# Optimization experiments

Measured on AMD Instinct MI355X. Metric: run time of the kernel, lower is better.

## Reference

```python
import jax, jax.numpy as jnp
import numpy as np

B, S, D = 2, 2048, 2048
H = 16
KV_RANK, Q_RANK = 512, 1536
NOPE, ROPE_D, VD = 128, 64, 128
QK_D = NOPE + ROPE_D  # 192


def _rope(t, positions):
    # t: (B, H, S, d) with d even; rotate-half RoPE, theta=10000
    d = t.shape[-1]
    inv_freq = 1.0 / (10000.0 ** (jnp.arange(0, d, 2, dtype=jnp.float32) / d))
    ang = positions.astype(jnp.float32)[:, None] * inv_freq  # (S, d//2)
    cos, sin = jnp.cos(ang), jnp.sin(ang)                    # (S, d//2)
    t1, t2 = t[..., : d // 2], t[..., d // 2 :]
    return jnp.concatenate([t1 * cos - t2 * sin, t2 * cos + t1 * sin], axis=-1)


def setup_inputs() -> dict:
    key = jax.random.key(0)
    ks = jax.random.split(key, 10)
    sc = 0.02
    return {
        "x": jax.random.normal(ks[0], (B, S, D), dtype=jnp.float32),
        "positions": jnp.arange(S, dtype=jnp.int32),
        # torch.nn.Linear weights are (out_features, in_features)
        "Wq_down": jax.random.normal(ks[1], (Q_RANK, D), dtype=jnp.float32) * sc,
        "Wq_up": jax.random.normal(ks[2], (H * NOPE, Q_RANK), dtype=jnp.float32) * sc,
        "Wq_rope": jax.random.normal(ks[3], (H * ROPE_D, Q_RANK), dtype=jnp.float32) * sc,
        "Wkv_down": jax.random.normal(ks[4], (KV_RANK, D), dtype=jnp.float32) * sc,
        "Wk_up": jax.random.normal(ks[5], (H * NOPE, KV_RANK), dtype=jnp.float32) * sc,
        "Wv_up": jax.random.normal(ks[6], (H * VD, KV_RANK), dtype=jnp.float32) * sc,
        "Wk_rope": jax.random.normal(ks[7], (ROPE_D, D), dtype=jnp.float32) * sc,
        "Wo": jax.random.normal(ks[8], (D, H * VD), dtype=jnp.float32) * sc,
    }


def reference(x, positions, Wq_down, Wq_up, Wq_rope, Wkv_down, Wk_up, Wv_up, Wk_rope, Wo):
    bsz, seq_len, _ = x.shape

    # Query path: low-rank down, then nope + rope up-projections
    c_q = x @ Wq_down.T                                             # (B, S, Q_RANK)
    q_c = (c_q @ Wq_up.T).reshape(bsz, seq_len, H, NOPE).transpose(0, 2, 1, 3)
    q_r = (c_q @ Wq_rope.T).reshape(bsz, seq_len, H, ROPE_D).transpose(0, 2, 1, 3)
    q_r = _rope(q_r, positions)
    q = jnp.concatenate([q_c, q_r], axis=-1)                        # (B, H, S, QK_D)

    # KV path: shared latent, single rope head broadcast to all heads
    c_kv = x @ Wkv_down.T                                           # (B, S, KV_RANK)
    k_c = (c_kv @ Wk_up.T).reshape(bsz, seq_len, H, NOPE).transpose(0, 2, 1, 3)
    v_c = (c_kv @ Wv_up.T).reshape(bsz, seq_len, H, VD).transpose(0, 2, 1, 3)
    k_r = (x @ Wk_rope.T).reshape(bsz, seq_len, 1, ROPE_D).transpose(0, 2, 1, 3)
    k_r = _rope(k_r, positions)
    k_r = jnp.broadcast_to(k_r, (bsz, H, seq_len, ROPE_D))
    k = jnp.concatenate([k_c, k_r], axis=-1)                        # (B, H, S, QK_D)

    # Causal SDPA, scale = 1/sqrt(total qk head dim)
    scale = 1.0 / math.sqrt(QK_D) if False else QK_D ** -0.5
    scores = jnp.einsum("bhqd,bhkd->bhqk", q, k) * scale
    causal = jnp.tril(jnp.ones((seq_len, seq_len), dtype=bool))
    scores = jnp.where(causal, scores, jnp.finfo(scores.dtype).min)
    attn = jax.nn.softmax(scores, axis=-1)
    out = jnp.einsum("bhqk,bhkd->bhqd", attn, v_c)                  # (B, H, S, VD)

    out = out.transpose(0, 2, 1, 3).reshape(bsz, seq_len, H * VD)
    return out @ Wo.T                                               # (B, S, D)
```

## Files before the change

### kernel.cpp

```cpp
#include <hip/hip_runtime.h>
#include <cmath>

#define SLEN 2048

typedef __bf16 bf16x8 __attribute__((ext_vector_type(8)));
typedef float  f32x4  __attribute__((ext_vector_type(4)));

__device__ inline void gld16(const void* g, void* l) {
    __builtin_amdgcn_global_load_lds(
        (const __attribute__((address_space(1))) void*)(uintptr_t)g,
        (__attribute__((address_space(3))) void*)(unsigned)(uintptr_t)l, 16, 0, 0);
}

struct CvArgs {
    const float* src[9];
    __bf16*      dst[9];
    long         cum[10];
};
__global__ __launch_bounds__(256)
void convert_all(CvArgs a) {
    long i8 = ((long)blockIdx.x * 256 + threadIdx.x) * 8;
    if (i8 >= a.cum[9]) return;
    int s = 0;
#pragma unroll
    for (int k = 1; k < 9; k++) if (i8 >= a.cum[k]) s = k;
    long loc = i8 - a.cum[s];
    const float* sp = a.src[s] + loc;
    float4 u0 = *(const float4*)(sp);
    float4 u1 = *(const float4*)(sp + 4);
    bf16x8 o;
    o[0] = (__bf16)u0.x; o[1] = (__bf16)u0.y; o[2] = (__bf16)u0.z; o[3] = (__bf16)u0.w;
    o[4] = (__bf16)u1.x; o[5] = (__bf16)u1.y; o[6] = (__bf16)u1.z; o[7] = (__bf16)u1.w;
    *(bf16x8*)(a.dst[s] + loc) = o;
}

struct Outs { __bf16* a; __bf16* b; __bf16* c; float* f; };

__global__ __launch_bounds__(256, 2)
void gemm_nt(const __bf16* __restrict__ A, const __bf16* __restrict__ B,
             Outs o, const int* __restrict__ positions,
             int M, int N, int K, int mode, float scale) {
    __shared__ __bf16 As[128 * 64];
    __shared__ __bf16 Bs[128 * 64];
    int tid = threadIdx.x;
    int wave = tid >> 6, lane = tid & 63;
    int lane15 = lane & 15, quad = lane >> 4;
    int ri = lane >> 3, ci = lane & 7;
    int cg = ci ^ ri;
    int m0 = blockIdx.x * 128, n0 = blockIdx.y * 128;
    int wm = (wave & 1) * 64, wn = (wave >> 1) * 64;
    f32x4 acc[4][4] = {};

    for (int k0 = 0; k0 < K; k0 += 64) {
#pragma unroll
        for (int t = 0; t < 4; t++) {
            int rr = wave * 32 + t * 8;
            int r = rr + ri;
            gld16(A + (size_t)(m0 + r) * K + k0 + cg * 8, As + rr * 64);
            int br = n0 + r; if (br > N - 1) br = N - 1;
            gld16(B + (size_t)br * K + k0 + cg * 8, Bs + rr * 64);
        }
        __syncthreads();
#pragma unroll
        for (int kk = 0; kk < 64; kk += 32) {
            int jb = kk >> 3;
            bf16x8 af[4], bfr[4];
#pragma unroll
            for (int mt = 0; mt < 4; mt++) {
                int rA = wm + mt * 16 + lane15;
                af[mt] = *(bf16x8*)(As + rA * 64 + (((jb + quad) ^ (rA & 7)) << 3));
            }
#pragma unroll
            for (int nt = 0; nt < 4; nt++) {
                int rB = wn + nt * 16 + lane15;
                bfr[nt] = *(bf16x8*)(Bs + rB * 64 + (((jb + quad) ^ (rB & 7)) << 3));
            }
#pragma unroll
            for (int mt = 0; mt < 4; mt++)
#pragma unroll
                for (int nt = 0; nt < 4; nt++)
                    acc[mt][nt] = __builtin_amdgcn_mfma_f32_16x16x32_bf16(
                        af[mt], bfr[nt], acc[mt][nt], 0, 0, 0);
        }
        __syncthreads();
    }

    const float KLOG = 13.287712379549449f / 32.0f;

    if (mode == 8 && n0 == 2048) {
        if (wn == 0) {
#pragma unroll
            for (int mt = 0; mt < 4; mt++) {
                int row = m0 + wm + mt * 16 + quad * 4;
#pragma unroll
                for (int nt = 0; nt < 2; nt++) {
                    int i = nt * 16 + lane15;
                    float inv = exp2f(-(float)i * KLOG);
#pragma unroll
                    for (int r = 0; r < 4; r++) {
                        int tok = row + r;
                        float p = (float)positions[tok & (SLEN - 1)];
                        float sn, cs; sincosf(p * inv, &sn, &cs);
                        float t1 = acc[mt][nt][r], t2 = acc[mt][nt + 2][r];
                        float rot1 = t1 * cs - t2 * sn;
                        float rot2 = t2 * cs + t1 * sn;
                        size_t ob = (size_t)tok * 3072 + 128;
#pragma unroll
                        for (int hh = 0; hh < 16; hh++) {
                            o.c[ob + hh * 192 + i]      = (__bf16)rot1;
                            o.c[ob + hh * 192 + 32 + i] = (__bf16)rot2;
                        }
                    }
                }
            }
        }
        return;
    }
    if (mode == 9 && n0 >= 2048) {
        int hh = (n0 + wn - 2048) >> 6;
#pragma unroll
        for (int mt = 0; mt < 4; mt++) {
            int row = m0 + wm + mt * 16 + quad * 4;
#pragma unroll
            for (int nt = 0; nt < 2; nt++) {
                int i = nt * 16 + lane15;
                float inv = exp2f(-(float)i * KLOG);
#pragma unroll
                for (int r = 0; r < 4; r++) {
                    int tok = row + r;
                    float p = (float)positions[tok & (SLEN - 1)];
                    float sn, cs; sincosf(p * inv, &sn, &cs);
                    float t1 = acc[mt][nt][r], t2 = acc[mt][nt + 2][r];
                    size_t ob = (size_t)tok * 3072 + hh * 192 + 128;
                    o.a[ob + i]      = (__bf16)((t1 * cs - t2 * sn) * scale);
                    o.a[ob + 32 + i] = (__bf16)((t2 * cs + t1 * sn) * scale);
                }
            }
        }
        return;
    }

#pragma unroll
    for (int mt = 0; mt < 4; mt++) {
        int row = m0 + wm + mt * 16 + quad * 4;
#pragma unroll
        for (int nt = 0; nt < 4; nt++) {
            int col = n0 + wn + nt * 16 + lane15;
            if (col < N) {
#pragma unroll
                for (int r = 0; r < 4; r++) {
                    float v = acc[mt][nt][r];
                    size_t rw = (size_t)(row + r);
                    if (mode == 2) {
                        o.f[rw * N + col] = v;
                    } else if (mode == 8) {
                        if (col < 1536) o.a[rw * 1536 + col] = (__bf16)v;
                        else            o.b[rw * 512 + col - 1536] = (__bf16)v;
                    } else if (mode == 9) {
                        o.a[rw * 3072 + (col >> 7) * 192 + (col & 127)] =
                            (__bf16)(v * scale);
                    } else {
                        if (col < 2048)
                            o.a[rw * 3072 + (col >> 7) * 192 + (col & 127)] = (__bf16)v;
                        else {
                            int d = col - 2048;
                            o.b[((size_t)d * 2 + (rw >> 11)) * 2048 + (rw & 2047)] = (__bf16)v;
                        }
                    }
                }
            }
        }
    }
}

__global__ __launch_bounds__(256, 2)
void mla_attn(const __bf16* __restrict__ Q, const __bf16* __restrict__ K,
              const __bf16* __restrict__ Vt, __bf16* __restrict__ O) {
    __shared__ __bf16 Ks[64 * 192];
    __shared__ __bf16 Vs[128 * 64];
    __shared__ __bf16 Ps[4][32][72];
    int tid = threadIdx.x, wave = tid >> 6, lane = tid & 63;
    int lane15 = lane & 15, quad = lane >> 4;
    int h = blockIdx.y, b = blockIdx.z;
    int x = blockIdx.x;
    int qt0 = (x & 1) ? (x >> 1) : (15 - (x >> 1));
    int qt = b ? (15 - qt0) : qt0;
    int q0 = qt * 128;
    const __bf16* Qb  = Q + (size_t)b * SLEN * 3072 + h * 192;
    const __bf16* Kb  = K + (size_t)b * SLEN * 3072 + h * 192;
    const __bf16* vtb = Vt + ((size_t)(h * 128) * 2 + b) * 2048;

    bf16x8 qf[2][6];
#pragma unroll
    for (int mt = 0; mt < 2; mt++) {
        int qrow = q0 + wave * 32 + mt * 16 + lane15;
#pragma unroll
        for (int kk = 0; kk < 6; kk++)
            qf[mt][kk] = *(const bf16x8*)(Qb + (size_t)qrow * 3072 + kk * 32 + quad * 8);
    }
    bf16x8 ones;
#pragma unroll
    for (int e = 0; e < 8; e++) ones[e] = (__bf16)1.0f;

    f32x4 o_acc[2][8] = {};
    float m_i[2][4], l_i[2][4];
#pragma unroll
    for (int mt = 0; mt < 2; mt++)
#pragma unroll
        for (int r = 0; r < 4; r++) { m_i[mt][r] = -3.0e38f; l_i[mt][r] = 0.0f; }

    for (int j0 = 0; j0 <= q0 + 64; j0 += 64) {
#pragma unroll
        for (int t = 0; t < 6; t++) {
            int sb = (wave * 6 + t) * 64;
            int slot = sb + lane;
            int r = slot / 24;
            int c = slot - r * 24;
            int cgk = (c & ~7) | ((c & 7) ^ (r & 7));
            gld16(Kb + (size_t)(j0 + r) * 3072 + cgk * 8, Ks + sb * 8);
        }
#pragma unroll
        for (int t = 0; t < 4; t++) {
            int sb = (wave * 4 + t) * 64;
            int slot = sb + lane;
            int r = slot >> 3, c = slot & 7;
            gld16(vtb + (size_t)r * 4096 + j0 + (c ^ (r & 7)) * 8, Vs + sb * 8);
        }
        __syncthreads();

        f32x4 acc[2][4] = {};
#pragma unroll
        for (int kk = 0; kk < 6; kk++) {
#pragma unroll
            for (int nt = 0; nt < 4; nt++) {
                int n = nt * 16 + lane15;
                int j = kk * 4 + quad;
                int cl = (j & ~7) | ((j & 7) ^ (n & 7));
                bf16x8 kf = *(bf16x8*)(Ks + n * 192 + cl * 8);
#pragma unroll
                for (int mt = 0; mt < 2; mt++)
                    acc[mt][nt] = __builtin_amdgcn_mfma_f32_16x16x32_bf16(
                        qf[mt][kk], kf, acc[mt][nt], 0, 0, 0);
            }
        }

        if (j0 >= q0) {
#pragma unroll
            for (int mt = 0; mt < 2; mt++) {
                int rowg = q0 + wave * 32 + mt * 16 + quad * 4;
#pragma unroll
                for (int nt = 0; nt < 4; nt++) {
                    int colg = j0 + nt * 16 + lane15;
#pragma unroll
                    for (int r = 0; r < 4; r++)
                        if (colg > rowg + r) acc[mt][nt][r] = -3.0e38f;
                }
            }
        }

        float mx[2][4];
        bool need = false;
#pragma unroll
        for (int mt = 0; mt < 2; mt++)
#pragma unroll
            for (int r = 0; r < 4; r++) {
                float v = fmaxf(fmaxf(acc[mt][0][r], acc[mt][1][r]),
                                fmaxf(acc[mt][2][r], acc[mt][3][r]));
                mx[mt][r] = v;
                need = need || (v > m_i[mt][r] + 24.0f);
            }
        if (__any(need)) {
#pragma unroll
            for (int mt = 0; mt < 2; mt++)
#pragma unroll
                for (int r = 0; r < 4; r++) {
                    float v = mx[mt][r];
#pragma unroll
                    for (int d = 8; d >= 1; d >>= 1) v = fmaxf(v, __shfl_xor(v, d));
                    float mn = fmaxf(m_i[mt][r], v);
                    float alpha = exp2f(m_i[mt][r] - mn);
                    m_i[mt][r] = mn;
                    l_i[mt][r] *= alpha;
#pragma unroll
                    for (int nt = 0; nt < 8; nt++) o_acc[mt][nt][r] *= alpha;
                }
        }

#pragma unroll
        for (int mt = 0; mt < 2; mt++)
#pragma unroll
            for (int r = 0; r < 4; r++)
#pragma unroll
                for (int nt = 0; nt < 4; nt++) {
                    float pp = exp2f(acc[mt][nt][r] - m_i[mt][r]);
                    Ps[wave][mt * 16 + quad * 4 + r][nt * 16 + lane15] = (__bf16)pp;
                }

        f32x4 rs[2] = {};
#pragma unroll
        for (int ks = 0; ks < 2; ks++) {
            bf16x8 pf[2];
#pragma unroll
            for (int mt = 0; mt < 2; mt++)
                pf[mt] = *(bf16x8*)(&Ps[wave][mt * 16 + lane15][ks * 32 + quad * 8]);
#pragma unroll
            for (int nt = 0; nt < 8; nt++) {
                int nn = nt * 16 + lane15;
                int j = ks * 4 + quad;
                bf16x8 vf = *(bf16x8*)(Vs + nn * 64 + (j ^ (nn & 7)) * 8);
#pragma unroll
                for (int mt = 0; mt < 2; mt++)
                    o_acc[mt][nt] = __builtin_amdgcn_mfma_f32_16x16x32_bf16(
                        pf[mt], vf, o_acc[mt][nt], 0, 0, 0);
            }
#pragma unroll
            for (int mt = 0; mt < 2; mt++)
                rs[mt] = __builtin_amdgcn_mfma_f32_16x16x32_bf16(
                    pf[mt], ones, rs[mt], 0, 0, 0);
        }
#pragma unroll
        for (int mt = 0; mt < 2; mt++)
#pragma unroll
            for (int r = 0; r < 4; r++) l_i[mt][r] += rs[mt][r];
        __syncthreads();
    }

    int tokb = b * SLEN + q0 + wave * 32 + quad * 4;
#pragma unroll
    for (int mt = 0; mt < 2; mt++) {
#pragma unroll
        for (int r = 0; r < 4; r++) {
            float inv_l = 1.0f / l_i[mt][r];
            int tok = tokb + mt * 16 + r;
#pragma unroll
            for (int nt = 0; nt < 8; nt++) {
                O[(size_t)tok * 2048 + h * 128 + nt * 16 + lane15] =
                    (__bf16)(o_acc[mt][nt][r] * inv_l);
            }
        }
    }
}

extern "C" void kernel_launch(void* const* d_in, const int* in_sizes, int n_in,
                              void* d_out, int out_size, void* d_ws, size_t ws_size,
                              hipStream_t stream) {
    (void)in_sizes; (void)n_in; (void)out_size; (void)ws_size;
    const int* pos = (const int*)d_in[1];
    float* out = (float*)d_out;

    char* ws = (char*)d_ws;
    size_t off = 0;
    auto alloc = [&](size_t bytes) {
        char* p = ws + off;
        off += (bytes + 255) & ~(size_t)255;
        return p;
    };
    __bf16* x_bf  = (__bf16*)alloc(8388608ull * 2);
    __bf16* Wcat1 = (__bf16*)alloc(4325376ull * 2);
    __bf16* Wcat2 = (__bf16*)alloc(4718592ull * 2);
    __bf16* Wcat3 = (__bf16*)alloc(4194304ull * 2);
    __bf16* Wob   = (__bf16*)alloc(4194304ull * 2);
    __bf16* c_q   = (__bf16*)alloc(4096ull * 1536 * 2);
    __bf16* c_kv  = (__bf16*)alloc(4096ull * 512 * 2);
    __bf16* v_t   = (__bf16*)alloc(4096ull * 2048 * 2);
    __bf16* q_all = (__bf16*)alloc(4096ull * 3072 * 2);
    __bf16* k_all = (__bf16*)alloc(4096ull * 3072 * 2);
    __bf16* attn_o = (__bf16*)c_q;

    const float scale_l2 = 1.4426950408889634f / sqrtf(192.0f);
    dim3 blk(256);

    CvArgs cv;
    cv.src[0] = (const float*)d_in[0]; cv.dst[0] = x_bf;
    cv.src[1] = (const float*)d_in[2]; cv.dst[1] = Wcat1;
    cv.src[2] = (const float*)d_in[5]; cv.dst[2] = Wcat1 + 3145728;
    cv.src[3] = (const float*)d_in[8]; cv.dst[3] = Wcat1 + 4194304;
    cv.src[4] = (const float*)d_in[3]; cv.dst[4] = Wcat2;
    cv.src[5] = (const float*)d_in[4]; cv.dst[5] = Wcat2 + 3145728;
    cv.src[6] = (const float*)d_in[6]; cv.dst[6] = Wcat3;
    cv.src[7] = (const float*)d_in[7]; cv.dst[7] = Wcat3 + 1048576;
    cv.src[8] = (const float*)d_in[9]; cv.dst[8] = Wob;
    long ns[9] = {8388608, 3145728, 1048576, 131072, 3145728, 1572864,
                  1048576, 1048576, 4194304};
    cv.cum[0] = 0;
    for (int i = 0; i < 9; i++) cv.cum[i + 1] = cv.cum[i] + ns[i];
    convert_all<<<dim3((unsigned)(cv.cum[9] / 2048)), blk, 0, stream>>>(cv);

    Outs o1 = { c_q, c_kv, k_all, nullptr };
    gemm_nt<<<dim3(32, 17), blk, 0, stream>>>(x_bf, Wcat1, o1, pos, 4096, 2112, 2048, 8, 1.0f);
    Outs o2 = { q_all, nullptr, nullptr, nullptr };
    gemm_nt<<<dim3(32, 24), blk, 0, stream>>>(c_q, Wcat2, o2, pos, 4096, 3072, 1536, 9, scale_l2);
    Outs o3 = { k_all, v_t, nullptr, nullptr };
    gemm_nt<<<dim3(32, 32), blk, 0, stream>>>(c_kv, Wcat3, o3, pos, 4096, 4096, 512, 10, 1.0f);
    mla_attn<<<dim3(16, 16, 2), blk, 0, stream>>>(q_all, k_all, v_t, attn_o);
    Outs o4 = { nullptr, nullptr, nullptr, out };
    gemm_nt<<<dim3(32, 16), blk, 0, stream>>>(attn_o, Wob, o4, pos, 4096, 2048, 2048, 2, 1.0f);
}
```

Before: 419.8 us.

## Double-buffer K/V tiles and pair causal query tiles per attention block

The attention kernel now double-buffers K and V in shared memory, prefetching the next 64-key tile while the current one is computed, and uses vmcnt waits with raw barriers in place of a full __syncthreads per tile. Each block processes two query tiles (x and 15-x) so every block gets an equal amount of causal work, and the grid is halved. Launch bounds drop to one block per CU, because the doubled LDS use and the extra registers cost occupancy that the prefetch is meant to make up for.

```diff
diff --git a/kernel.cpp b/kernel.cpp
--- a/kernel.cpp
+++ b/kernel.cpp
@@ -173,43 +173,25 @@
     }
 }
 
-__global__ __launch_bounds__(256, 2)
+__global__ __launch_bounds__(256, 1)
 void mla_attn(const __bf16* __restrict__ Q, const __bf16* __restrict__ K,
               const __bf16* __restrict__ Vt, __bf16* __restrict__ O) {
-    __shared__ __bf16 Ks[64 * 192];
-    __shared__ __bf16 Vs[128 * 64];
+    __shared__ __bf16 Ks[2][64 * 192];
+    __shared__ __bf16 Vs[2][128 * 64];
     __shared__ __bf16 Ps[4][32][72];
     int tid = threadIdx.x, wave = tid >> 6, lane = tid & 63;
     int lane15 = lane & 15, quad = lane >> 4;
     int h = blockIdx.y, b = blockIdx.z;
     int x = blockIdx.x;
-    int qt0 = (x & 1) ? (x >> 1) : (15 - (x >> 1));
-    int qt = b ? (15 - qt0) : qt0;
-    int q0 = qt * 128;
     const __bf16* Qb  = Q + (size_t)b * SLEN * 3072 + h * 192;
     const __bf16* Kb  = K + (size_t)b * SLEN * 3072 + h * 192;
     const __bf16* vtb = Vt + ((size_t)(h * 128) * 2 + b) * 2048;
 
-    bf16x8 qf[2][6];
-#pragma unroll
-    for (int mt = 0; mt < 2; mt++) {
-        int qrow = q0 + wave * 32 + mt * 16 + lane15;
-#pragma unroll
-        for (int kk = 0; kk < 6; kk++)
-            qf[mt][kk] = *(const bf16x8*)(Qb + (size_t)qrow * 3072 + kk * 32 + quad * 8);
-    }
     bf16x8 ones;
 #pragma unroll
     for (int e = 0; e < 8; e++) ones[e] = (__bf16)1.0f;
 
-    f32x4 o_acc[2][8] = {};
-    float m_i[2][4], l_i[2][4];
-#pragma unroll
-    for (int mt = 0; mt < 2; mt++)
-#pragma unroll
-        for (int r = 0; r < 4; r++) { m_i[mt][r] = -3.0e38f; l_i[mt][r] = 0.0f; }
-
-    for (int j0 = 0; j0 <= q0 + 64; j0 += 64) {
+    auto stage = [&](int j0, int buf) {
 #pragma unroll
         for (int t = 0; t < 6; t++) {
             int sb = (wave * 6 + t) * 64;
@@ -217,125 +199,166 @@
             int r = slot / 24;
             int c = slot - r * 24;
             int cgk = (c & ~7) | ((c & 7) ^ (r & 7));
-            gld16(Kb + (size_t)(j0 + r) * 3072 + cgk * 8, Ks + sb * 8);
+            gld16(Kb + (size_t)(j0 + r) * 3072 + cgk * 8, &Ks[buf][0] + sb * 8);
         }
 #pragma unroll
         for (int t = 0; t < 4; t++) {
             int sb = (wave * 4 + t) * 64;
             int slot = sb + lane;
             int r = slot >> 3, c = slot & 7;
-            gld16(vtb + (size_t)r * 4096 + j0 + (c ^ (r & 7)) * 8, Vs + sb * 8);
-        }
-        __syncthreads();
-
-        f32x4 acc[2][4] = {};
-#pragma unroll
-        for (int kk = 0; kk < 6; kk++) {
-#pragma unroll
-            for (int nt = 0; nt < 4; nt++) {
-                int n = nt * 16 + lane15;
-                int j = kk * 4 + quad;
-                int cl = (j & ~7) | ((j & 7) ^ (n & 7));
-                bf16x8 kf = *(bf16x8*)(Ks + n * 192 + cl * 8);
+            gld16(vtb + (size_t)r * 4096 + j0 + (c ^ (r & 7)) * 8, &Vs[buf][0] + sb * 8);
+        }
+    };
+
+    for (int pass = 0; pass < 2; pass++) {
+        int qt = pass ? (15 - x) : x;
+        int q0 = qt * 128;
+
+        bf16x8 qf[2][6];
+#pragma unroll
+        for (int mt = 0; mt < 2; mt++) {
+            int qrow = q0 + wave * 32 + mt * 16 + lane15;
+#pragma unroll
+            for (int kk = 0; kk < 6; kk++)
+                qf[mt][kk] = *(const bf16x8*)(Qb + (size_t)qrow * 3072 + kk * 32 + quad * 8);
+        }
+
+        f32x4 o_acc[2][8] = {};
+        float m_i[2][4], l_i[2][4];
+#pragma unroll
+        for (int mt = 0; mt < 2; mt++)
+#pragma unroll
+            for (int r = 0; r < 4; r++) { m_i[mt][r] = -3.0e38f; l_i[mt][r] = 0.0f; }
+
+        int ntiles = 2 * qt + 2;
+        stage(0, 0);
+
+        for (int t = 0; t < ntiles; t++) {
+            int cur = t & 1;
+            if (t + 1 < ntiles) {
+                stage((t + 1) * 64, cur ^ 1);
+                asm volatile("s_waitcnt vmcnt(10)" ::: "memory");
+            } else {
+                asm volatile("s_waitcnt vmcnt(0)" ::: "memory");
+            }
+            __builtin_amdgcn_sched_barrier(0);
+            __builtin_amdgcn_s_barrier();
+            __builtin_amdgcn_sched_barrier(0);
+
+            const __bf16* Ksc = &Ks[cur][0];
+            const __bf16* Vsc = &Vs[cur][0];
+            int j0 = t * 64;
+
+            f32x4 acc[2][4] = {};
+#pragma unroll
+            for (int kk = 0; kk < 6; kk++) {
+#pragma unroll
+                for (int nt = 0; nt < 4; nt++) {
+                    int n = nt * 16 + lane15;
+                    int j = kk * 4 + quad;
+                    int cl = (j & ~7) | ((j & 7) ^ (n & 7));
+                    bf16x8 kf = *(bf16x8*)(Ksc + n * 192 + cl * 8);
+#pragma unroll
+                    for (int mt = 0; mt < 2; mt++)
+                        acc[mt][nt] = __builtin_amdgcn_mfma_f32_16x16x32_bf16(
+                            qf[mt][kk], kf, acc[mt][nt], 0, 0, 0);
+                }
+            }
+
+            if (j0 >= q0) {
+#pragma unroll
+                for (int mt = 0; mt < 2; mt++) {
+                    int rowg = q0 + wave * 32 + mt * 16 + quad * 4;
+#pragma unroll
+                    for (int nt = 0; nt < 4; nt++) {
+                        int colg = j0 + nt * 16 + lane15;
+#pragma unroll
+                        for (int r = 0; r < 4; r++)
+                            if (colg > rowg + r) acc[mt][nt][r] = -3.0e38f;
+                    }
+                }
+            }
+
+            float mx[2][4];
+            bool need = false;
+#pragma unroll
+            for (int mt = 0; mt < 2; mt++)
+#pragma unroll
+                for (int r = 0; r < 4; r++) {
+                    float v = fmaxf(fmaxf(acc[mt][0][r], acc[mt][1][r]),
+                                    fmaxf(acc[mt][2][r], acc[mt][3][r]));
+                    mx[mt][r] = v;
+                    need = need || (v > m_i[mt][r] + 24.0f);
+                }
+            if (__any(need)) {
 #pragma unroll
                 for (int mt = 0; mt < 2; mt++)
-                    acc[mt][nt] = __builtin_amdgcn_mfma_f32_16x16x32_bf16(
-                        qf[mt][kk], kf, acc[mt][nt], 0, 0, 0);
-            }
-        }
-
-        if (j0 >= q0) {
-#pragma unroll
-            for (int mt = 0; mt < 2; mt++) {
-                int rowg = q0 + wave * 32 + mt * 16 + quad * 4;
-#pragma unroll
-                for (int nt = 0; nt < 4; nt++) {
-                    int colg = j0 + nt * 16 + lane15;
-#pragma unroll
-                    for (int r = 0; r < 4; r++)
-                        if (colg > rowg + r) acc[mt][nt][r] = -3.0e38f;
-                }
-            }
-        }
-
-        float mx[2][4];
-        bool need = false;
-#pragma unroll
-        for (int mt = 0; mt < 2; mt++)
+#pragma unroll
+                    for (int r = 0; r < 4; r++) {
+                        float v = mx[mt][r];
+#pragma unroll
+                        for (int d = 8; d >= 1; d >>= 1) v = fmaxf(v, __shfl_xor(v, d));
+                        float mn = fmaxf(m_i[mt][r], v);
+                        float alpha = exp2f(m_i[mt][r] - mn);
+                        m_i[mt][r] = mn;
+                        l_i[mt][r] *= alpha;
+#pragma unroll
+                        for (int nt = 0; nt < 8; nt++) o_acc[mt][nt][r] *= alpha;
+                    }
+            }
+
+#pragma unroll
+            for (int mt = 0; mt < 2; mt++)
+#pragma unroll
+                for (int r = 0; r < 4; r++)
+#pragma unroll
+                    for (int nt = 0; nt < 4; nt++) {
+                        float pp = exp2f(acc[mt][nt][r] - m_i[mt][r]);
+                        Ps[wave][mt * 16 + quad * 4 + r][nt * 16 + lane15] = (__bf16)pp;
+                    }
+
+            f32x4 rs[2] = {};
+#pragma unroll
+            for (int ks = 0; ks < 2; ks++) {
+                bf16x8 pf[2];
+#pragma unroll
+                for (int mt = 0; mt < 2; mt++)
+                    pf[mt] = *(bf16x8*)(&Ps[wave][mt * 16 + lane15][ks * 32 + quad * 8]);
+#pragma unroll
+                for (int nt = 0; nt < 8; nt++) {
+                    int nn = nt * 16 + lane15;
+                    int j = ks * 4 + quad;
+                    bf16x8 vf = *(bf16x8*)(Vsc + nn * 64 + (j ^ (nn & 7)) * 8);
+#pragma unroll
+                    for (int mt = 0; mt < 2; mt++)
+                        o_acc[mt][nt] = __builtin_amdgcn_mfma_f32_16x16x32_bf16(
+                            pf[mt], vf, o_acc[mt][nt], 0, 0, 0);
+                }
+#pragma unroll
+                for (int mt = 0; mt < 2; mt++)
+                    rs[mt] = __builtin_amdgcn_mfma_f32_16x16x32_bf16(
+                        pf[mt], ones, rs[mt], 0, 0, 0);
+            }
+#pragma unroll
+            for (int mt = 0; mt < 2; mt++)
+#pragma unroll
+                for (int r = 0; r < 4; r++) l_i[mt][r] += rs[mt][r];
+
+            __builtin_amdgcn_s_barrier();
+        }
+
+        int tokb = b * SLEN + q0 + wave * 32 + quad * 4;
+#pragma unroll
+        for (int mt = 0; mt < 2; mt++) {
 #pragma unroll
             for (int r = 0; r < 4; r++) {
-                float v = fmaxf(fmaxf(acc[mt][0][r], acc[mt][1][r]),
-                                fmaxf(acc[mt][2][r], acc[mt][3][r]));
-                mx[mt][r] = v;
-                need = need || (v > m_i[mt][r] + 24.0f);
-            }
-        if (__any(need)) {
-#pragma unroll
-            for (int mt = 0; mt < 2; mt++)
-#pragma unroll
-                for (int r = 0; r < 4; r++) {
-                    float v = mx[mt][r];
-#pragma unroll
-                    for (int d = 8; d >= 1; d >>= 1) v = fmaxf(v, __shfl_xor(v, d));
-                    float mn = fmaxf(m_i[mt][r], v);
-                    float alpha = exp2f(m_i[mt][r] - mn);
-                    m_i[mt][r] = mn;
-                    l_i[mt][r] *= alpha;
-#pragma unroll
-                    for (int nt = 0; nt < 8; nt++) o_acc[mt][nt][r] *= alpha;
-                }
-        }
-
-#pragma unroll
-        for (int mt = 0; mt < 2; mt++)
-#pragma unroll
-            for (int r = 0; r < 4; r++)
-#pragma unroll
-                for (int nt = 0; nt < 4; nt++) {
-                    float pp = exp2f(acc[mt][nt][r] - m_i[mt][r]);
-                    Ps[wave][mt * 16 + quad * 4 + r][nt * 16 + lane15] = (__bf16)pp;
-                }
-
-        f32x4 rs[2] = {};
-#pragma unroll
-        for (int ks = 0; ks < 2; ks++) {
-            bf16x8 pf[2];
-#pragma unroll
-            for (int mt = 0; mt < 2; mt++)
-                pf[mt] = *(bf16x8*)(&Ps[wave][mt * 16 + lane15][ks * 32 + quad * 8]);
-#pragma unroll
-            for (int nt = 0; nt < 8; nt++) {
-                int nn = nt * 16 + lane15;
-                int j = ks * 4 + quad;
-                bf16x8 vf = *(bf16x8*)(Vs + nn * 64 + (j ^ (nn & 7)) * 8);
-#pragma unroll
-                for (int mt = 0; mt < 2; mt++)
-                    o_acc[mt][nt] = __builtin_amdgcn_mfma_f32_16x16x32_bf16(
-                        pf[mt], vf, o_acc[mt][nt], 0, 0, 0);
-            }
-#pragma unroll
-            for (int mt = 0; mt < 2; mt++)
-                rs[mt] = __builtin_amdgcn_mfma_f32_16x16x32_bf16(
-                    pf[mt], ones, rs[mt], 0, 0, 0);
-        }
-#pragma unroll
-        for (int mt = 0; mt < 2; mt++)
-#pragma unroll
-            for (int r = 0; r < 4; r++) l_i[mt][r] += rs[mt][r];
-        __syncthreads();
-    }
-
-    int tokb = b * SLEN + q0 + wave * 32 + quad * 4;
-#pragma unroll
-    for (int mt = 0; mt < 2; mt++) {
-#pragma unroll
-        for (int r = 0; r < 4; r++) {
-            float inv_l = 1.0f / l_i[mt][r];
-            int tok = tokb + mt * 16 + r;
-#pragma unroll
-            for (int nt = 0; nt < 8; nt++) {
-                O[(size_t)tok * 2048 + h * 128 + nt * 16 + lane15] =
-                    (__bf16)(o_acc[mt][nt][r] * inv_l);
+                float inv_l = 1.0f / l_i[mt][r];
+                int tok = tokb + mt * 16 + r;
+#pragma unroll
+                for (int nt = 0; nt < 8; nt++) {
+                    O[(size_t)tok * 2048 + h * 128 + nt * 16 + lane15] =
+                        (__bf16)(o_acc[mt][nt][r] * inv_l);
+                }
             }
         }
     }
@@ -392,7 +415,7 @@
     gemm_nt<<<dim3(32, 24), blk, 0, stream>>>(c_q, Wcat2, o2, pos, 4096, 3072, 1536, 9, scale_l2);
     Outs o3 = { k_all, v_t, nullptr, nullptr };
     gemm_nt<<<dim3(32, 32), blk, 0, stream>>>(c_kv, Wcat3, o3, pos, 4096, 4096, 512, 10, 1.0f);
-    mla_attn<<<dim3(16, 16, 2), blk, 0, stream>>>(q_all, k_all, v_t, attn_o);
+    mla_attn<<<dim3(8, 16, 2), blk, 0, stream>>>(q_all, k_all, v_t, attn_o);
     Outs o4 = { nullptr, nullptr, nullptr, out };
     gemm_nt<<<dim3(32, 16), blk, 0, stream>>>(attn_o, Wob, o4, pos, 4096, 2048, 2048, 2, 1.0f);
 }
```

Result: slower. 432.7 us (+3.1%).
